# Kernel tuning notes

Hardware: AMD Instinct MI355X
Metric: run time of the kernel (lower is better)

## Reference

```python
import jax, jax.numpy as jnp
import numpy as np

B, C, D = 16, 128, 256


def setup_inputs() -> dict:
    key = jax.random.key(0)
    ks = jax.random.split(key, 12)
    s = 0.05
    return {
        "h_t": jax.random.normal(ks[0], (B, C, D), jnp.float32),
        "A_a": jax.random.normal(ks[1], (C, C), jnp.float32) * s,
        "A_m": jax.random.normal(ks[2], (C, C), jnp.float32) * s,
        "W1": jax.random.normal(ks[3], (2 * D, D), jnp.float32) * s,
        "b1": jax.random.normal(ks[4], (D,), jnp.float32) * s,
        "W2": jax.random.normal(ks[5], (D, 1), jnp.float32) * s,
        "b2": jax.random.normal(ks[6], (1,), jnp.float32) * s,
        "Wa": jax.random.normal(ks[7], (D, D), jnp.float32) * s,
        "ba": jax.random.normal(ks[8], (D,), jnp.float32) * s,
        "Wm": jax.random.normal(ks[9], (D, D), jnp.float32) * s,
        "bm": jax.random.normal(ks[10], (D,), jnp.float32) * s,
        "beta1": jnp.float32(1.0),
        "beta2": jnp.float32(1.0),
        "beta3": jnp.float32(1.0),
    }


def reference(h_t, A_a, A_m, W1, b1, W2, b2, Wa, ba, Wm, bm, beta1, beta2, beta3):
    d = h_t.shape[-1]
    # Pairwise edge-MLP score S[b,u,v] = sigmoid(W2 @ relu(W1 @ [h_u; h_v] + b1) + b2).
    # Split W1 into the half acting on h_u and the half acting on h_v, so the
    # (B,C,C,2D) concat never materializes (same math as Linear on the concat).
    pre_u = jnp.einsum('bud,dk->buk', h_t, W1[:d])        # (B,C,D)
    pre_v = jnp.einsum('bvd,dk->bvk', h_t, W1[d:])        # (B,C,D)
    hidden = jax.nn.relu(pre_u[:, :, None, :] + pre_v[:, None, :, :] + b1)  # (B,C,C,D)
    S = jax.nn.sigmoid(jnp.einsum('buvk,ko->buvo', hidden, W2)[..., 0] + b2[0])  # (B,C,C)

    # Additive aggregation: a_t[b,v,:] = sum_u (S*A_a)[b,u,v] * h_t[b,u,:]
    a_t = jnp.einsum('buv,bud->bvd', S * A_a, h_t)

    # Hadamard aggregation: m_t[b,v,d] = sum_u A_m[u,v] * h[b,u,d] * h[b,v,d]
    #                              = (A_m^T @ h_t) * h_t  (avoids (B,C,C,D) tensor)
    m_t = jnp.einsum('uv,bud->bvd', A_m, h_t) * h_t

    z_t = (beta1 * h_t
           + beta2 * (jnp.einsum('bvd,de->bve', a_t, Wa) + ba)
           + beta3 * (jnp.einsum('bvd,de->bve', m_t, Wm) + bm))
    return z_t
```

## Files before the change

kernel.cpp:

```cpp
#include <hip/hip_runtime.h>
#include <hip/hip_bf16.h>

#define B_ 16
#define C_ 128
#define D_ 256

typedef unsigned int uint32;
typedef unsigned short u16;
typedef __attribute__((ext_vector_type(8))) short s8v;
typedef __attribute__((ext_vector_type(4))) float f4v;

__device__ __forceinline__ u16 bfu(float x) {
  union { __hip_bfloat16 h; u16 s; } u;
  u.h = __float2bfloat16(x);
  return u.s;
}
__device__ __forceinline__ float2 bf2x(uint32 x) {
  return make_float2(__uint_as_float(x << 16), __uint_as_float(x & 0xffff0000u));
}

__global__ __launch_bounds__(256) void kprep(const float* __restrict__ h,
    const float* __restrict__ W1, const float* __restrict__ Wa,
    const float* __restrict__ Wm, const float* __restrict__ Am,
    const float* __restrict__ ba, const float* __restrict__ bm,
    const float* __restrict__ be2, const float* __restrict__ be3,
    u16* __restrict__ hb, u16* __restrict__ hbT, u16* __restrict__ w1t,
    u16* __restrict__ wcatT, u16* __restrict__ amT, float* __restrict__ bcat) {
  const int blk = blockIdx.x;
  const int tid = threadIdx.x;
  if (blk < 512) {
    const int i4 = (blk * 256 + tid) * 4;
    const float4 v = *(const float4*)(h + i4);
    ushort4 o; o.x = bfu(v.x); o.y = bfu(v.y); o.z = bfu(v.z); o.w = bfu(v.w);
    *(ushort4*)(hb + i4) = o;
  } else if (blk < 1024) {
    const int i4 = ((blk - 512) * 256 + tid) * 4;
    const int b = i4 >> 15;
    const int r = i4 & 32767;
    const int d = r >> 7, u0 = r & 127;
    const float x0 = h[(b * C_ + u0 + 0) * D_ + d];
    const float x1 = h[(b * C_ + u0 + 1) * D_ + d];
    const float x2 = h[(b * C_ + u0 + 2) * D_ + d];
    const float x3 = h[(b * C_ + u0 + 3) * D_ + d];
    ushort4 o; o.x = bfu(x0); o.y = bfu(x1); o.z = bfu(x2); o.w = bfu(x3);
    *(ushort4*)(hbT + i4) = o;
  } else if (blk < 1152) {
    const int i4 = ((blk - 1024) * 256 + tid) * 4;
    const int n = i4 >> 8, k0 = i4 & 255;
    float x0, x1, x2, x3;
    if (n < 256) {
      x0 = W1[(k0 + 0) * 256 + n]; x1 = W1[(k0 + 1) * 256 + n];
      x2 = W1[(k0 + 2) * 256 + n]; x3 = W1[(k0 + 3) * 256 + n];
    } else {
      const int nn = n - 256;
      x0 = W1[(256 + k0 + 0) * 256 + nn]; x1 = W1[(256 + k0 + 1) * 256 + nn];
      x2 = W1[(256 + k0 + 2) * 256 + nn]; x3 = W1[(256 + k0 + 3) * 256 + nn];
    }
    ushort4 o; o.x = bfu(x0); o.y = bfu(x1); o.z = bfu(x2); o.w = bfu(x3);
    *(ushort4*)(w1t + i4) = o;
  } else if (blk < 1280) {
    const float b2v = be2[0], b3v = be3[0];
    const int i4 = ((blk - 1152) * 256 + tid) * 4;
    const int n = i4 >> 9, k0 = i4 & 511;
    float x0, x1, x2, x3;
    if (k0 < 256) {
      x0 = b2v * Wa[(k0 + 0) * 256 + n]; x1 = b2v * Wa[(k0 + 1) * 256 + n];
      x2 = b2v * Wa[(k0 + 2) * 256 + n]; x3 = b2v * Wa[(k0 + 3) * 256 + n];
    } else {
      const int kk = k0 - 256;
      x0 = b3v * Wm[(kk + 0) * 256 + n]; x1 = b3v * Wm[(kk + 1) * 256 + n];
      x2 = b3v * Wm[(kk + 2) * 256 + n]; x3 = b3v * Wm[(kk + 3) * 256 + n];
    }
    ushort4 o; o.x = bfu(x0); o.y = bfu(x1); o.z = bfu(x2); o.w = bfu(x3);
    *(ushort4*)(wcatT + i4) = o;
  } else if (blk < 1296) {
    const int i4 = ((blk - 1280) * 256 + tid) * 4;
    const int v = i4 >> 7, u0 = i4 & 127;
    const float x0 = Am[(u0 + 0) * C_ + v];
    const float x1 = Am[(u0 + 1) * C_ + v];
    const float x2 = Am[(u0 + 2) * C_ + v];
    const float x3 = Am[(u0 + 3) * C_ + v];
    ushort4 o; o.x = bfu(x0); o.y = bfu(x1); o.z = bfu(x2); o.w = bfu(x3);
    *(ushort4*)(amT + i4) = o;
  } else {
    const float b2v = be2[0], b3v = be3[0];
    bcat[tid] = b2v * ba[tid] + b3v * bm[tid];
  }
}

__global__ __launch_bounds__(256) void k1_mfma(const u16* __restrict__ hb,
    const u16* __restrict__ w1t, const float* __restrict__ b1,
    u16* __restrict__ P, u16* __restrict__ Q) {
  const int lane = threadIdx.x & 63;
  const int w = blockIdx.x * 4 + (threadIdx.x >> 6);
  const int nt = w & 31, mt = w >> 5;
  const int row0 = mt * 16, col0 = nt * 16;
  const int lr = lane & 15, lk = lane >> 4;
  const u16* ap = hb + (row0 + lr) * D_ + lk * 8;
  const u16* bp = w1t + (col0 + lr) * D_ + lk * 8;
  f4v acc = {0.f, 0.f, 0.f, 0.f};
#pragma unroll
  for (int ks = 0; ks < 8; ++ks) {
    const s8v af = *(const s8v*)(ap + ks * 32);
    const s8v bf = *(const s8v*)(bp + ks * 32);
    acc = __builtin_amdgcn_mfma_f32_16x16x32_bf16(af, bf, acc, 0, 0, 0);
  }
  const int col = col0 + lr;
  if (col0 < 256) {
#pragma unroll
    for (int r = 0; r < 4; ++r)
      P[(row0 + lk * 4 + r) * D_ + col] = bfu(acc[r]);
  } else {
    const float bb = b1[col - 256];
#pragma unroll
    for (int r = 0; r < 4; ++r)
      Q[(row0 + lk * 4 + r) * D_ + (col - 256)] = bfu(acc[r] + bb);
  }
}

__global__ __launch_bounds__(256) void k2_s(const u16* __restrict__ P,
    const u16* __restrict__ Q, const float* __restrict__ W2,
    const float* __restrict__ b2, const float* __restrict__ Aa,
    u16* __restrict__ SA) {
  const int b = blockIdx.z;
  const int u0 = blockIdx.x * 16;
  const int v0 = blockIdx.y * 16;
  const int tid = threadIdx.x;
  __shared__ uint32 Pl[16][130];
  __shared__ uint32 Ql[16][130];
  const uint32* Pg = (const uint32*)(P + (b * C_ + u0) * D_);
  const uint32* Qg = (const uint32*)(Q + (b * C_ + v0) * D_);
  {
    const int r = tid >> 5;
    const int c4 = (tid & 31) * 4;
#pragma unroll
    for (int half = 0; half < 2; ++half) {
      const int rr = r + half * 8;
      const uint4 pv = *(const uint4*)&Pg[rr * 128 + c4];
      const uint4 qv = *(const uint4*)&Qg[rr * 128 + c4];
      *(uint2*)&Pl[rr][c4]     = make_uint2(pv.x, pv.y);
      *(uint2*)&Pl[rr][c4 + 2] = make_uint2(pv.z, pv.w);
      *(uint2*)&Ql[rr][c4]     = make_uint2(qv.x, qv.y);
      *(uint2*)&Ql[rr][c4 + 2] = make_uint2(qv.z, qv.w);
    }
  }
  __syncthreads();
  const int ul = tid & 15;
  const int vl = tid >> 4;
  const float4* __restrict__ w4 = (const float4*)W2;
  float a0 = 0.f, a1 = 0.f;
#pragma unroll 8
  for (int kk = 0; kk < 128; kk += 2) {
    const uint2 pu = *(const uint2*)&Pl[ul][kk];
    const uint2 qu = *(const uint2*)&Ql[vl][kk];
    const float4 wv = w4[kk >> 1];
    const float2 p0 = bf2x(pu.x), p1 = bf2x(pu.y);
    const float2 q0 = bf2x(qu.x), q1 = bf2x(qu.y);
    a0 = fmaf(fmaxf(p0.x + q0.x, 0.f), wv.x, a0);
    a0 = fmaf(fmaxf(p0.y + q0.y, 0.f), wv.y, a0);
    a1 = fmaf(fmaxf(p1.x + q1.x, 0.f), wv.z, a1);
    a1 = fmaf(fmaxf(p1.y + q1.y, 0.f), wv.w, a1);
  }
  const float s = 1.f / (1.f + __expf(-(a0 + a1 + b2[0])));
  const int u = u0 + ul, v = v0 + vl;
  SA[b * C_ * C_ + v * C_ + u] = bfu(s * Aa[u * C_ + v]);
}

__global__ __launch_bounds__(256) void k3_mfma(const u16* __restrict__ SA,
    const u16* __restrict__ amT, const u16* __restrict__ hbT,
    const float* __restrict__ h, u16* __restrict__ atcat) {
  const int lane = threadIdx.x & 63;
  const int w = blockIdx.x * 4 + (threadIdx.x >> 6);
  const int bt = w >> 7, rem = w & 127;
  const int mt = rem >> 4, nt = rem & 15;
  const int v0 = mt * 16, d0 = nt * 16;
  const int lr = lane & 15, lk = lane >> 4;
  const u16* sap = SA + (bt * C_ + v0 + lr) * C_ + lk * 8;
  const u16* a2p = amT + (v0 + lr) * C_ + lk * 8;
  const u16* bp = hbT + (bt * D_ + d0 + lr) * C_ + lk * 8;
  f4v acca = {0.f, 0.f, 0.f, 0.f}, accm = {0.f, 0.f, 0.f, 0.f};
#pragma unroll
  for (int ks = 0; ks < 4; ++ks) {
    const s8v a1 = *(const s8v*)(sap + ks * 32);
    const s8v a2 = *(const s8v*)(a2p + ks * 32);
    const s8v bf = *(const s8v*)(bp + ks * 32);
    acca = __builtin_amdgcn_mfma_f32_16x16x32_bf16(a1, bf, acca, 0, 0, 0);
    accm = __builtin_amdgcn_mfma_f32_16x16x32_bf16(a2, bf, accm, 0, 0, 0);
  }
  const int d = d0 + lr;
#pragma unroll
  for (int r = 0; r < 4; ++r) {
    const int grow = bt * C_ + v0 + lk * 4 + r;
    atcat[grow * 512 + d] = bfu(acca[r]);
    const float hv = h[grow * D_ + d];
    atcat[grow * 512 + 256 + d] = bfu(accm[r] * hv);
  }
}

__global__ __launch_bounds__(256) void k4_mfma(const u16* __restrict__ atcat,
    const u16* __restrict__ wcatT, const float* __restrict__ bcat,
    const float* __restrict__ h, const float* __restrict__ be1,
    float* __restrict__ z) {
  const int lane = threadIdx.x & 63;
  const int w = blockIdx.x * 4 + (threadIdx.x >> 6);
  const int nt = w & 15, mt = w >> 4;
  const int row0 = mt * 16, col0 = nt * 16;
  const int lr = lane & 15, lk = lane >> 4;
  const u16* ap = atcat + (row0 + lr) * 512 + lk * 8;
  const u16* bp = wcatT + (col0 + lr) * 512 + lk * 8;
  f4v acc = {0.f, 0.f, 0.f, 0.f};
#pragma unroll
  for (int ks = 0; ks < 16; ++ks) {
    const s8v af = *(const s8v*)(ap + ks * 32);
    const s8v bf = *(const s8v*)(bp + ks * 32);
    acc = __builtin_amdgcn_mfma_f32_16x16x32_bf16(af, bf, acc, 0, 0, 0);
  }
  const float b1v = be1[0];
  const int col = col0 + lr;
  const float bc = bcat[col];
#pragma unroll
  for (int r = 0; r < 4; ++r) {
    const int row = row0 + lk * 4 + r;
    z[row * D_ + col] = acc[r] + b1v * h[row * D_ + col] + bc;
  }
}

extern "C" void kernel_launch(void* const* d_in, const int* in_sizes, int n_in,
                              void* d_out, int out_size, void* d_ws, size_t ws_size,
                              hipStream_t stream) {
  const float* h   = (const float*)d_in[0];
  const float* Aa  = (const float*)d_in[1];
  const float* Am  = (const float*)d_in[2];
  const float* W1  = (const float*)d_in[3];
  const float* b1  = (const float*)d_in[4];
  const float* W2  = (const float*)d_in[5];
  const float* b2  = (const float*)d_in[6];
  const float* Wa  = (const float*)d_in[7];
  const float* ba  = (const float*)d_in[8];
  const float* Wm  = (const float*)d_in[9];
  const float* bm  = (const float*)d_in[10];
  const float* be1 = (const float*)d_in[11];
  const float* be2 = (const float*)d_in[12];
  const float* be3 = (const float*)d_in[13];
  float* z = (float*)d_out;

  char* wsb = (char*)d_ws;
  u16*   hb    = (u16*)(wsb);
  u16*   hbT   = (u16*)(wsb + (1 << 20));
  u16*   w1t   = (u16*)(wsb + (2 << 20));
  u16*   wcatT = (u16*)(wsb + (2 << 20) + (256 << 10));
  u16*   amT   = (u16*)(wsb + (2 << 20) + (512 << 10));
  float* bcat  = (float*)(wsb + (2 << 20) + (544 << 10));
  u16*   P     = (u16*)(wsb + (3 << 20));
  u16*   Q     = (u16*)(wsb + (4 << 20));
  u16*   SA    = (u16*)(wsb + (5 << 20));
  u16*   atcat = (u16*)(wsb + (6 << 20));

  kprep  <<<1297, 256, 0, stream>>>(h, W1, Wa, Wm, Am, ba, bm, be2, be3,
                                    hb, hbT, w1t, wcatT, amT, bcat);
  k1_mfma<<<1024, 256, 0, stream>>>(hb, w1t, b1, P, Q);
  k2_s   <<<dim3(8, 8, 16), 256, 0, stream>>>(P, Q, W2, b2, Aa, SA);
  k3_mfma<<<512, 256, 0, stream>>>(SA, amT, hbT, h, atcat);
  k4_mfma<<<512, 256, 0, stream>>>(atcat, wcatT, bcat, h, be1, z);
}
```

Baseline: 121.2 us.

## Fuse all stages into one cooperative persistent kernel with grid syncs

Replaces five separate launches with a single cooperative kernel of 512 blocks that steps through prep, the W1 projection, the pairwise score and the aggregation plus output stages, separated by grid.sync. The bf16 copy of h is dropped: the first projection converts fp32 h to bf16 on the fly. The aggregation and final projection are fused per block through a swizzled LDS tile, so the atcat intermediate never goes to global memory. This removes launch gaps and intermediate traffic, but adds grid barrier cost and leaves the last stage running on only 128 of the 512 blocks.

Measured after the change: 329.2 us. +171.5%, slower.

```diff
diff --git a/kernel.cpp b/kernel.cpp
--- a/kernel.cpp
+++ b/kernel.cpp
@@ -1,9 +1,12 @@
 #include <hip/hip_runtime.h>
+#include <hip/hip_cooperative_groups.h>
 #include <hip/hip_bf16.h>
 
 #define B_ 16
 #define C_ 128
 #define D_ 256
+
+namespace cg = cooperative_groups;
 
 typedef unsigned int uint32;
 typedef unsigned short u16;
@@ -19,209 +22,218 @@
   return make_float2(__uint_as_float(x << 16), __uint_as_float(x & 0xffff0000u));
 }
 
-__global__ __launch_bounds__(256) void kprep(const float* __restrict__ h,
-    const float* __restrict__ W1, const float* __restrict__ Wa,
-    const float* __restrict__ Wm, const float* __restrict__ Am,
-    const float* __restrict__ ba, const float* __restrict__ bm,
+__global__ __launch_bounds__(256, 2) void kfused(
+    const float* __restrict__ h,  const float* __restrict__ Aa,
+    const float* __restrict__ Am, const float* __restrict__ W1,
+    const float* __restrict__ b1, const float* __restrict__ W2,
+    const float* __restrict__ b2, const float* __restrict__ Wa,
+    const float* __restrict__ ba, const float* __restrict__ Wm,
+    const float* __restrict__ bm, const float* __restrict__ be1,
     const float* __restrict__ be2, const float* __restrict__ be3,
-    u16* __restrict__ hb, u16* __restrict__ hbT, u16* __restrict__ w1t,
-    u16* __restrict__ wcatT, u16* __restrict__ amT, float* __restrict__ bcat) {
-  const int blk = blockIdx.x;
+    float* __restrict__ z,
+    u16* __restrict__ w1t, u16* __restrict__ wcatT, u16* __restrict__ amT,
+    float* __restrict__ bcat, u16* __restrict__ hbT,
+    u16* __restrict__ P, u16* __restrict__ Q, u16* __restrict__ SA) {
+  cg::grid_group grid = cg::this_grid();
+  const int bid = blockIdx.x;
   const int tid = threadIdx.x;
-  if (blk < 512) {
-    const int i4 = (blk * 256 + tid) * 4;
-    const float4 v = *(const float4*)(h + i4);
-    ushort4 o; o.x = bfu(v.x); o.y = bfu(v.y); o.z = bfu(v.z); o.w = bfu(v.w);
-    *(ushort4*)(hb + i4) = o;
-  } else if (blk < 1024) {
-    const int i4 = ((blk - 512) * 256 + tid) * 4;
-    const int b = i4 >> 15;
-    const int r = i4 & 32767;
-    const int d = r >> 7, u0 = r & 127;
-    const float x0 = h[(b * C_ + u0 + 0) * D_ + d];
-    const float x1 = h[(b * C_ + u0 + 1) * D_ + d];
-    const float x2 = h[(b * C_ + u0 + 2) * D_ + d];
-    const float x3 = h[(b * C_ + u0 + 3) * D_ + d];
-    ushort4 o; o.x = bfu(x0); o.y = bfu(x1); o.z = bfu(x2); o.w = bfu(x3);
-    *(ushort4*)(hbT + i4) = o;
-  } else if (blk < 1152) {
-    const int i4 = ((blk - 1024) * 256 + tid) * 4;
-    const int n = i4 >> 8, k0 = i4 & 255;
-    float x0, x1, x2, x3;
-    if (n < 256) {
-      x0 = W1[(k0 + 0) * 256 + n]; x1 = W1[(k0 + 1) * 256 + n];
-      x2 = W1[(k0 + 2) * 256 + n]; x3 = W1[(k0 + 3) * 256 + n];
+
+  __shared__ union SmT {
+    struct { uint32 Pl[16][130]; uint32 Ql[16][130]; } s2;
+    u16 at[16 * 512];
+  } sm;
+
+  for (int t = bid; t < 785; t += 512) {
+    if (t < 512) {
+      const int i4 = (t * 256 + tid) * 4;
+      const int b = i4 >> 15, r = i4 & 32767, d = r >> 7, u0 = r & 127;
+      ushort4 o;
+      o.x = bfu(h[(b * C_ + u0 + 0) * D_ + d]);
+      o.y = bfu(h[(b * C_ + u0 + 1) * D_ + d]);
+      o.z = bfu(h[(b * C_ + u0 + 2) * D_ + d]);
+      o.w = bfu(h[(b * C_ + u0 + 3) * D_ + d]);
+      *(ushort4*)(hbT + i4) = o;
+    } else if (t < 640) {
+      const int i4 = ((t - 512) * 256 + tid) * 4;
+      const int n = i4 >> 8, k0 = i4 & 255;
+      float x0, x1, x2, x3;
+      if (n < 256) {
+        x0 = W1[(k0 + 0) * 256 + n]; x1 = W1[(k0 + 1) * 256 + n];
+        x2 = W1[(k0 + 2) * 256 + n]; x3 = W1[(k0 + 3) * 256 + n];
+      } else {
+        const int nn = n - 256;
+        x0 = W1[(256 + k0 + 0) * 256 + nn]; x1 = W1[(256 + k0 + 1) * 256 + nn];
+        x2 = W1[(256 + k0 + 2) * 256 + nn]; x3 = W1[(256 + k0 + 3) * 256 + nn];
+      }
+      ushort4 o; o.x = bfu(x0); o.y = bfu(x1); o.z = bfu(x2); o.w = bfu(x3);
+      *(ushort4*)(w1t + i4) = o;
+    } else if (t < 768) {
+      const float b2v = be2[0], b3v = be3[0];
+      const int i4 = ((t - 640) * 256 + tid) * 4;
+      const int n = i4 >> 9, k0 = i4 & 511;
+      float x0, x1, x2, x3;
+      if (k0 < 256) {
+        x0 = b2v * Wa[(k0 + 0) * 256 + n]; x1 = b2v * Wa[(k0 + 1) * 256 + n];
+        x2 = b2v * Wa[(k0 + 2) * 256 + n]; x3 = b2v * Wa[(k0 + 3) * 256 + n];
+      } else {
+        const int kk = k0 - 256;
+        x0 = b3v * Wm[(kk + 0) * 256 + n]; x1 = b3v * Wm[(kk + 1) * 256 + n];
+        x2 = b3v * Wm[(kk + 2) * 256 + n]; x3 = b3v * Wm[(kk + 3) * 256 + n];
+      }
+      ushort4 o; o.x = bfu(x0); o.y = bfu(x1); o.z = bfu(x2); o.w = bfu(x3);
+      *(ushort4*)(wcatT + i4) = o;
+    } else if (t < 784) {
+      const int i4 = ((t - 768) * 256 + tid) * 4;
+      const int v = i4 >> 7, u0 = i4 & 127;
+      ushort4 o;
+      o.x = bfu(Am[(u0 + 0) * C_ + v]);
+      o.y = bfu(Am[(u0 + 1) * C_ + v]);
+      o.z = bfu(Am[(u0 + 2) * C_ + v]);
+      o.w = bfu(Am[(u0 + 3) * C_ + v]);
+      *(ushort4*)(amT + i4) = o;
     } else {
-      const int nn = n - 256;
-      x0 = W1[(256 + k0 + 0) * 256 + nn]; x1 = W1[(256 + k0 + 1) * 256 + nn];
-      x2 = W1[(256 + k0 + 2) * 256 + nn]; x3 = W1[(256 + k0 + 3) * 256 + nn];
-    }
-    ushort4 o; o.x = bfu(x0); o.y = bfu(x1); o.z = bfu(x2); o.w = bfu(x3);
-    *(ushort4*)(w1t + i4) = o;
-  } else if (blk < 1280) {
-    const float b2v = be2[0], b3v = be3[0];
-    const int i4 = ((blk - 1152) * 256 + tid) * 4;
-    const int n = i4 >> 9, k0 = i4 & 511;
-    float x0, x1, x2, x3;
-    if (k0 < 256) {
-      x0 = b2v * Wa[(k0 + 0) * 256 + n]; x1 = b2v * Wa[(k0 + 1) * 256 + n];
-      x2 = b2v * Wa[(k0 + 2) * 256 + n]; x3 = b2v * Wa[(k0 + 3) * 256 + n];
-    } else {
-      const int kk = k0 - 256;
-      x0 = b3v * Wm[(kk + 0) * 256 + n]; x1 = b3v * Wm[(kk + 1) * 256 + n];
-      x2 = b3v * Wm[(kk + 2) * 256 + n]; x3 = b3v * Wm[(kk + 3) * 256 + n];
-    }
-    ushort4 o; o.x = bfu(x0); o.y = bfu(x1); o.z = bfu(x2); o.w = bfu(x3);
-    *(ushort4*)(wcatT + i4) = o;
-  } else if (blk < 1296) {
-    const int i4 = ((blk - 1280) * 256 + tid) * 4;
-    const int v = i4 >> 7, u0 = i4 & 127;
-    const float x0 = Am[(u0 + 0) * C_ + v];
-    const float x1 = Am[(u0 + 1) * C_ + v];
-    const float x2 = Am[(u0 + 2) * C_ + v];
-    const float x3 = Am[(u0 + 3) * C_ + v];
-    ushort4 o; o.x = bfu(x0); o.y = bfu(x1); o.z = bfu(x2); o.w = bfu(x3);
-    *(ushort4*)(amT + i4) = o;
-  } else {
-    const float b2v = be2[0], b3v = be3[0];
-    bcat[tid] = b2v * ba[tid] + b3v * bm[tid];
-  }
-}
-
-__global__ __launch_bounds__(256) void k1_mfma(const u16* __restrict__ hb,
-    const u16* __restrict__ w1t, const float* __restrict__ b1,
-    u16* __restrict__ P, u16* __restrict__ Q) {
-  const int lane = threadIdx.x & 63;
-  const int w = blockIdx.x * 4 + (threadIdx.x >> 6);
-  const int nt = w & 31, mt = w >> 5;
-  const int row0 = mt * 16, col0 = nt * 16;
-  const int lr = lane & 15, lk = lane >> 4;
-  const u16* ap = hb + (row0 + lr) * D_ + lk * 8;
-  const u16* bp = w1t + (col0 + lr) * D_ + lk * 8;
-  f4v acc = {0.f, 0.f, 0.f, 0.f};
-#pragma unroll
-  for (int ks = 0; ks < 8; ++ks) {
-    const s8v af = *(const s8v*)(ap + ks * 32);
-    const s8v bf = *(const s8v*)(bp + ks * 32);
-    acc = __builtin_amdgcn_mfma_f32_16x16x32_bf16(af, bf, acc, 0, 0, 0);
-  }
-  const int col = col0 + lr;
-  if (col0 < 256) {
-#pragma unroll
-    for (int r = 0; r < 4; ++r)
-      P[(row0 + lk * 4 + r) * D_ + col] = bfu(acc[r]);
-  } else {
-    const float bb = b1[col - 256];
-#pragma unroll
-    for (int r = 0; r < 4; ++r)
-      Q[(row0 + lk * 4 + r) * D_ + (col - 256)] = bfu(acc[r] + bb);
-  }
-}
-
-__global__ __launch_bounds__(256) void k2_s(const u16* __restrict__ P,
-    const u16* __restrict__ Q, const float* __restrict__ W2,
-    const float* __restrict__ b2, const float* __restrict__ Aa,
-    u16* __restrict__ SA) {
-  const int b = blockIdx.z;
-  const int u0 = blockIdx.x * 16;
-  const int v0 = blockIdx.y * 16;
-  const int tid = threadIdx.x;
-  __shared__ uint32 Pl[16][130];
-  __shared__ uint32 Ql[16][130];
-  const uint32* Pg = (const uint32*)(P + (b * C_ + u0) * D_);
-  const uint32* Qg = (const uint32*)(Q + (b * C_ + v0) * D_);
+      bcat[tid] = be2[0] * ba[tid] + be3[0] * bm[tid];
+    }
+  }
+  grid.sync();
+
   {
-    const int r = tid >> 5;
-    const int c4 = (tid & 31) * 4;
-#pragma unroll
-    for (int half = 0; half < 2; ++half) {
-      const int rr = r + half * 8;
-      const uint4 pv = *(const uint4*)&Pg[rr * 128 + c4];
-      const uint4 qv = *(const uint4*)&Qg[rr * 128 + c4];
-      *(uint2*)&Pl[rr][c4]     = make_uint2(pv.x, pv.y);
-      *(uint2*)&Pl[rr][c4 + 2] = make_uint2(pv.z, pv.w);
-      *(uint2*)&Ql[rr][c4]     = make_uint2(qv.x, qv.y);
-      *(uint2*)&Ql[rr][c4 + 2] = make_uint2(qv.z, qv.w);
-    }
-  }
-  __syncthreads();
-  const int ul = tid & 15;
-  const int vl = tid >> 4;
-  const float4* __restrict__ w4 = (const float4*)W2;
-  float a0 = 0.f, a1 = 0.f;
+    const int lane = tid & 63;
+    const int lr = lane & 15, lk = lane >> 4;
+#pragma unroll
+    for (int rep = 0; rep < 2; ++rep) {
+      const int w = bid * 4 + (tid >> 6) + rep * 2048;
+      const int nt = w & 31, mt = w >> 5;
+      const int row0 = mt * 16, col0 = nt * 16;
+      const float* ap = h + (row0 + lr) * D_ + lk * 8;
+      const u16* bp = w1t + (col0 + lr) * D_ + lk * 8;
+      f4v acc = {0.f, 0.f, 0.f, 0.f};
+#pragma unroll
+      for (int ks = 0; ks < 8; ++ks) {
+        const float4 a0 = *(const float4*)(ap + ks * 32);
+        const float4 a1 = *(const float4*)(ap + ks * 32 + 4);
+        union { s8v v; u16 u[8]; } af;
+        af.u[0] = bfu(a0.x); af.u[1] = bfu(a0.y); af.u[2] = bfu(a0.z); af.u[3] = bfu(a0.w);
+        af.u[4] = bfu(a1.x); af.u[5] = bfu(a1.y); af.u[6] = bfu(a1.z); af.u[7] = bfu(a1.w);
+        const s8v bf = *(const s8v*)(bp + ks * 32);
+        acc = __builtin_amdgcn_mfma_f32_16x16x32_bf16(af.v, bf, acc, 0, 0, 0);
+      }
+      const int col = col0 + lr;
+      if (col0 < 256) {
+#pragma unroll
+        for (int r = 0; r < 4; ++r)
+          P[(row0 + lk * 4 + r) * D_ + col] = bfu(acc[r]);
+      } else {
+        const float bb = b1[col - 256];
+#pragma unroll
+        for (int r = 0; r < 4; ++r)
+          Q[(row0 + lk * 4 + r) * D_ + (col - 256)] = bfu(acc[r] + bb);
+      }
+    }
+  }
+  grid.sync();
+
+  {
+    const float4* __restrict__ w4 = (const float4*)W2;
+#pragma unroll
+    for (int rep = 0; rep < 2; ++rep) {
+      const int t = bid + rep * 512;
+      const int b = t >> 6;
+      const int u0 = ((t >> 3) & 7) * 16;
+      const int v0 = (t & 7) * 16;
+      const uint32* Pg = (const uint32*)(P + (b * C_ + u0) * D_);
+      const uint32* Qg = (const uint32*)(Q + (b * C_ + v0) * D_);
+      {
+        const int r = tid >> 5;
+        const int c4 = (tid & 31) * 4;
+#pragma unroll
+        for (int half = 0; half < 2; ++half) {
+          const int rr = r + half * 8;
+          const uint4 pv = *(const uint4*)&Pg[rr * 128 + c4];
+          const uint4 qv = *(const uint4*)&Qg[rr * 128 + c4];
+          *(uint2*)&sm.s2.Pl[rr][c4]     = make_uint2(pv.x, pv.y);
+          *(uint2*)&sm.s2.Pl[rr][c4 + 2] = make_uint2(pv.z, pv.w);
+          *(uint2*)&sm.s2.Ql[rr][c4]     = make_uint2(qv.x, qv.y);
+          *(uint2*)&sm.s2.Ql[rr][c4 + 2] = make_uint2(qv.z, qv.w);
+        }
+      }
+      __syncthreads();
+      const int ul = tid & 15;
+      const int vl = tid >> 4;
+      float a0 = 0.f, a1 = 0.f;
 #pragma unroll 8
-  for (int kk = 0; kk < 128; kk += 2) {
-    const uint2 pu = *(const uint2*)&Pl[ul][kk];
-    const uint2 qu = *(const uint2*)&Ql[vl][kk];
-    const float4 wv = w4[kk >> 1];
-    const float2 p0 = bf2x(pu.x), p1 = bf2x(pu.y);
-    const float2 q0 = bf2x(qu.x), q1 = bf2x(qu.y);
-    a0 = fmaf(fmaxf(p0.x + q0.x, 0.f), wv.x, a0);
-    a0 = fmaf(fmaxf(p0.y + q0.y, 0.f), wv.y, a0);
-    a1 = fmaf(fmaxf(p1.x + q1.x, 0.f), wv.z, a1);
-    a1 = fmaf(fmaxf(p1.y + q1.y, 0.f), wv.w, a1);
-  }
-  const float s = 1.f / (1.f + __expf(-(a0 + a1 + b2[0])));
-  const int u = u0 + ul, v = v0 + vl;
-  SA[b * C_ * C_ + v * C_ + u] = bfu(s * Aa[u * C_ + v]);
-}
-
-__global__ __launch_bounds__(256) void k3_mfma(const u16* __restrict__ SA,
-    const u16* __restrict__ amT, const u16* __restrict__ hbT,
-    const float* __restrict__ h, u16* __restrict__ atcat) {
-  const int lane = threadIdx.x & 63;
-  const int w = blockIdx.x * 4 + (threadIdx.x >> 6);
-  const int bt = w >> 7, rem = w & 127;
-  const int mt = rem >> 4, nt = rem & 15;
-  const int v0 = mt * 16, d0 = nt * 16;
-  const int lr = lane & 15, lk = lane >> 4;
-  const u16* sap = SA + (bt * C_ + v0 + lr) * C_ + lk * 8;
-  const u16* a2p = amT + (v0 + lr) * C_ + lk * 8;
-  const u16* bp = hbT + (bt * D_ + d0 + lr) * C_ + lk * 8;
-  f4v acca = {0.f, 0.f, 0.f, 0.f}, accm = {0.f, 0.f, 0.f, 0.f};
-#pragma unroll
-  for (int ks = 0; ks < 4; ++ks) {
-    const s8v a1 = *(const s8v*)(sap + ks * 32);
-    const s8v a2 = *(const s8v*)(a2p + ks * 32);
-    const s8v bf = *(const s8v*)(bp + ks * 32);
-    acca = __builtin_amdgcn_mfma_f32_16x16x32_bf16(a1, bf, acca, 0, 0, 0);
-    accm = __builtin_amdgcn_mfma_f32_16x16x32_bf16(a2, bf, accm, 0, 0, 0);
-  }
-  const int d = d0 + lr;
-#pragma unroll
-  for (int r = 0; r < 4; ++r) {
-    const int grow = bt * C_ + v0 + lk * 4 + r;
-    atcat[grow * 512 + d] = bfu(acca[r]);
-    const float hv = h[grow * D_ + d];
-    atcat[grow * 512 + 256 + d] = bfu(accm[r] * hv);
-  }
-}
-
-__global__ __launch_bounds__(256) void k4_mfma(const u16* __restrict__ atcat,
-    const u16* __restrict__ wcatT, const float* __restrict__ bcat,
-    const float* __restrict__ h, const float* __restrict__ be1,
-    float* __restrict__ z) {
-  const int lane = threadIdx.x & 63;
-  const int w = blockIdx.x * 4 + (threadIdx.x >> 6);
-  const int nt = w & 15, mt = w >> 4;
-  const int row0 = mt * 16, col0 = nt * 16;
-  const int lr = lane & 15, lk = lane >> 4;
-  const u16* ap = atcat + (row0 + lr) * 512 + lk * 8;
-  const u16* bp = wcatT + (col0 + lr) * 512 + lk * 8;
-  f4v acc = {0.f, 0.f, 0.f, 0.f};
-#pragma unroll
-  for (int ks = 0; ks < 16; ++ks) {
-    const s8v af = *(const s8v*)(ap + ks * 32);
-    const s8v bf = *(const s8v*)(bp + ks * 32);
-    acc = __builtin_amdgcn_mfma_f32_16x16x32_bf16(af, bf, acc, 0, 0, 0);
-  }
-  const float b1v = be1[0];
-  const int col = col0 + lr;
-  const float bc = bcat[col];
-#pragma unroll
-  for (int r = 0; r < 4; ++r) {
-    const int row = row0 + lk * 4 + r;
-    z[row * D_ + col] = acc[r] + b1v * h[row * D_ + col] + bc;
+      for (int kk = 0; kk < 128; kk += 2) {
+        const uint2 pu = *(const uint2*)&sm.s2.Pl[ul][kk];
+        const uint2 qu = *(const uint2*)&sm.s2.Ql[vl][kk];
+        const float4 wv = w4[kk >> 1];
+        const float2 p0 = bf2x(pu.x), p1 = bf2x(pu.y);
+        const float2 q0 = bf2x(qu.x), q1 = bf2x(qu.y);
+        a0 = fmaf(fmaxf(p0.x + q0.x, 0.f), wv.x, a0);
+        a0 = fmaf(fmaxf(p0.y + q0.y, 0.f), wv.y, a0);
+        a1 = fmaf(fmaxf(p1.x + q1.x, 0.f), wv.z, a1);
+        a1 = fmaf(fmaxf(p1.y + q1.y, 0.f), wv.w, a1);
+      }
+      const float s = 1.f / (1.f + __expf(-(a0 + a1 + b2[0])));
+      const int u = u0 + ul, v = v0 + vl;
+      SA[b * C_ * C_ + v * C_ + u] = bfu(s * Aa[u * C_ + v]);
+      __syncthreads();
+    }
+  }
+  grid.sync();
+
+  if (bid < 128) {
+    const int bt = bid >> 3;
+    const int v0 = (bid & 7) * 16;
+    const int lane = tid & 63, widx = tid >> 6;
+    const int lr = lane & 15, lk = lane >> 4;
+#pragma unroll
+    for (int i = 0; i < 4; ++i) {
+      const int d0 = (widx * 4 + i) * 16;
+      const u16* sap = SA + (bt * C_ + v0 + lr) * C_ + lk * 8;
+      const u16* a2p = amT + (v0 + lr) * C_ + lk * 8;
+      const u16* bp  = hbT + (bt * D_ + d0 + lr) * C_ + lk * 8;
+      f4v acca = {0.f, 0.f, 0.f, 0.f}, accm = {0.f, 0.f, 0.f, 0.f};
+#pragma unroll
+      for (int ks = 0; ks < 4; ++ks) {
+        const s8v a1 = *(const s8v*)(sap + ks * 32);
+        const s8v a2 = *(const s8v*)(a2p + ks * 32);
+        const s8v bf = *(const s8v*)(bp + ks * 32);
+        acca = __builtin_amdgcn_mfma_f32_16x16x32_bf16(a1, bf, acca, 0, 0, 0);
+        accm = __builtin_amdgcn_mfma_f32_16x16x32_bf16(a2, bf, accm, 0, 0, 0);
+      }
+      const int d = d0 + lr;
+#pragma unroll
+      for (int r = 0; r < 4; ++r) {
+        const int R = lk * 4 + r;
+        const int grow = bt * C_ + v0 + R;
+        const float hv = h[grow * D_ + d];
+        const int swz = (R & 7) << 4;
+        *(u16*)((char*)sm.at + R * 1024 + ((d * 2) ^ swz)) = bfu(acca[r]);
+        *(u16*)((char*)sm.at + R * 1024 + (((256 + d) * 2) ^ swz)) = bfu(accm[r] * hv);
+      }
+    }
+    __syncthreads();
+    const float b1v = be1[0];
+#pragma unroll
+    for (int i = 0; i < 4; ++i) {
+      const int col0 = (widx * 4 + i) * 16;
+      const u16* bp = wcatT + (col0 + lr) * 512 + lk * 8;
+      f4v acc = {0.f, 0.f, 0.f, 0.f};
+#pragma unroll
+      for (int ks = 0; ks < 16; ++ks) {
+        const int boff = lr * 1024 + ((ks * 64 + lk * 16) ^ ((lr & 7) << 4));
+        const s8v af = *(const s8v*)((char*)sm.at + boff);
+        const s8v bf = *(const s8v*)(bp + ks * 32);
+        acc = __builtin_amdgcn_mfma_f32_16x16x32_bf16(af, bf, acc, 0, 0, 0);
+      }
+      const int col = col0 + lr;
+      const float bc = bcat[col];
+#pragma unroll
+      for (int r = 0; r < 4; ++r) {
+        const int row = bt * C_ + v0 + lk * 4 + r;
+        z[row * D_ + col] = acc[r] + b1v * h[row * D_ + col] + bc;
+      }
+    }
   }
 }
 
@@ -245,21 +257,21 @@
   float* z = (float*)d_out;
 
   char* wsb = (char*)d_ws;
-  u16*   hb    = (u16*)(wsb);
+  u16*   w1t   = (u16*)(wsb);
+  u16*   wcatT = (u16*)(wsb + (256 << 10));
+  u16*   amT   = (u16*)(wsb + (512 << 10));
+  float* bcat  = (float*)(wsb + (544 << 10));
   u16*   hbT   = (u16*)(wsb + (1 << 20));
-  u16*   w1t   = (u16*)(wsb + (2 << 20));
-  u16*   wcatT = (u16*)(wsb + (2 << 20) + (256 << 10));
-  u16*   amT   = (u16*)(wsb + (2 << 20) + (512 << 10));
-  float* bcat  = (float*)(wsb + (2 << 20) + (544 << 10));
-  u16*   P     = (u16*)(wsb + (3 << 20));
-  u16*   Q     = (u16*)(wsb + (4 << 20));
-  u16*   SA    = (u16*)(wsb + (5 << 20));
-  u16*   atcat = (u16*)(wsb + (6 << 20));
-
-  kprep  <<<1297, 256, 0, stream>>>(h, W1, Wa, Wm, Am, ba, bm, be2, be3,
-                                    hb, hbT, w1t, wcatT, amT, bcat);
-  k1_mfma<<<1024, 256, 0, stream>>>(hb, w1t, b1, P, Q);
-  k2_s   <<<dim3(8, 8, 16), 256, 0, stream>>>(P, Q, W2, b2, Aa, SA);
-  k3_mfma<<<512, 256, 0, stream>>>(SA, amT, hbT, h, atcat);
-  k4_mfma<<<512, 256, 0, stream>>>(atcat, wcatT, bcat, h, be1, z);
-}
+  u16*   P     = (u16*)(wsb + (2 << 20));
+  u16*   Q     = (u16*)(wsb + (3 << 20));
+  u16*   SA    = (u16*)(wsb + (4 << 20));
+
+  void* args[] = {
+    (void*)&h, (void*)&Aa, (void*)&Am, (void*)&W1, (void*)&b1, (void*)&W2,
+    (void*)&b2, (void*)&Wa, (void*)&ba, (void*)&Wm, (void*)&bm, (void*)&be1,
+    (void*)&be2, (void*)&be3, (void*)&z, (void*)&w1t, (void*)&wcatT,
+    (void*)&amT, (void*)&bcat, (void*)&hbT, (void*)&P, (void*)&Q, (void*)&SA,
+  };
+  hipLaunchCooperativeKernel((const void*)kfused, dim3(512), dim3(256),
+                             args, 0, stream);
+}
```
